# Kernel optimization log

Hardware: AMD Instinct MI355X
Metric: run time of the kernel (lower is better)

The kernel has to match this reference:

```python
import jax, jax.numpy as jnp
import numpy as np

EPS = 1e-12  # F.normalize default eps

def setup_inputs() -> dict:
    key = jax.random.key(0)
    k1, k2, k3, k4, k5, k6 = jax.random.split(key, 6)
    B, N, F_in, F_out = 8, 2048, 128, 128
    h = jax.random.normal(k1, (B, N, F_in), dtype=jnp.float32)
    # binary adjacency with avg degree ~32 (p = 32/2048)
    adj = (jax.random.uniform(k2, (B, N, N)) < (32.0 / N)).astype(jnp.float32)
    lim = 1.0 / np.sqrt(F_in)
    W_self = jax.random.uniform(k3, (F_in, F_out), minval=-lim, maxval=lim, dtype=jnp.float32)
    b_self = jax.random.uniform(k4, (F_out,), minval=-lim, maxval=lim, dtype=jnp.float32)
    W_neigh = jax.random.uniform(k5, (F_in, F_out), minval=-lim, maxval=lim, dtype=jnp.float32)
    b_neigh = jax.random.uniform(k6, (F_out,), minval=-lim, maxval=lim, dtype=jnp.float32)
    return {"h": h, "adj": adj, "W_self": W_self, "b_self": b_self,
            "W_neigh": W_neigh, "b_neigh": b_neigh}

def reference(h, adj, W_self, b_self, W_neigh, b_neigh):
    # Original builds (B,N,N,F) = adj[:, i, :, None] * h then mean over dim=-2.
    # mean divides by N (not degree), so aggregated = (adj @ h) / N. Fused form:
    N = h.shape[1]
    aggregated = jnp.einsum('bij,bjf->bif', adj, h) / N  # (B,N,F_in)
    out = h @ W_self + b_self + aggregated @ W_neigh + b_neigh
    out = jax.nn.relu(out)
    # F.normalize(p=2, dim=-1): x / max(||x||, eps)
    norm = jnp.linalg.norm(out, axis=-1, keepdims=True)
    out = out / jnp.maximum(norm, EPS)
    return out  # dropout(p=0.0) is identity
```

## Files before the change

### kernel.cpp

```cpp
#include <hip/hip_runtime.h>

typedef unsigned int u32;
typedef unsigned long long u64;
typedef float f4v __attribute__((ext_vector_type(4)));
typedef float f2v __attribute__((ext_vector_type(2)));

#define BATCH 8
#define NNODE 2048
#define FEAT  128
#define CAP   320


#define APITCH 68
#define BPITCH 132

__global__ __launch_bounds__(256) void gemm_pg_kernel(
    const float* __restrict__ h,
    const float* __restrict__ Ws,
    const float* __restrict__ bs,
    const float* __restrict__ Wn,
    const float* __restrict__ bn,
    float* __restrict__ P,
    float* __restrict__ G)
{
  __shared__ float sA[64 * APITCH];
  __shared__ float sB[64 * BPITCH];

  const int tid = threadIdx.x;
  const int tx = tid & 15;
  const int rg = tid >> 4;
  const int r0 = blockIdx.x * 64;
  const int half = blockIdx.y;
  const float* __restrict__ W = half ? Wn : Ws;
  float* __restrict__ op = half ? G : P;

  float acc[4][8];
#pragma unroll
  for (int r = 0; r < 4; r++)
#pragma unroll
    for (int c = 0; c < 8; c++) acc[r][c] = 0.0f;

  const int arl = tid >> 2;
  const int aq  = tid & 3;
  const int bkl = tid >> 2;
  const int bq  = tid & 3;

  for (int t = 0; t < 2; t++) {
    __syncthreads();
    {
      const float* src = h + (size_t)(r0 + arl) * FEAT + t * 64 + aq * 4;
#pragma unroll
      for (int ii = 0; ii < 4; ii++) {
        float4 vv = *(const float4*)(src + ii * 16);
        int kk = aq * 4 + ii * 16;
        sA[(kk + 0) * APITCH + arl] = vv.x;
        sA[(kk + 1) * APITCH + arl] = vv.y;
        sA[(kk + 2) * APITCH + arl] = vv.z;
        sA[(kk + 3) * APITCH + arl] = vv.w;
      }
    }
    {
      const float* src = W + (size_t)(t * 64 + bkl) * FEAT;
#pragma unroll
      for (int j = 0; j < 8; j++) {
        int cw = (bq + 4 * j) * 4;
        *(float4*)&sB[bkl * BPITCH + cw] = *(const float4*)(src + cw);
      }
    }
    __syncthreads();
#pragma unroll 4
    for (int k = 0; k < 64; k++) {
      float4 av = *(const float4*)&sA[k * APITCH + rg * 4];
      float4 b0 = *(const float4*)&sB[k * BPITCH + tx * 8];
      float4 b1 = *(const float4*)&sB[k * BPITCH + tx * 8 + 4];
      const float a[4] = {av.x, av.y, av.z, av.w};
      const float bb[8] = {b0.x, b0.y, b0.z, b0.w, b1.x, b1.y, b1.z, b1.w};
#pragma unroll
      for (int r = 0; r < 4; r++)
#pragma unroll
        for (int c = 0; c < 8; c++)
          acc[r][c] += a[r] * bb[c];
    }
  }

  float bias[8];
  if (half == 0) {
    float4 b0 = *(const float4*)(bs + tx * 8);
    float4 b1 = *(const float4*)(bs + tx * 8 + 4);
    float4 c0 = *(const float4*)(bn + tx * 8);
    float4 c1 = *(const float4*)(bn + tx * 8 + 4);
    bias[0] = b0.x + c0.x; bias[1] = b0.y + c0.y;
    bias[2] = b0.z + c0.z; bias[3] = b0.w + c0.w;
    bias[4] = b1.x + c1.x; bias[5] = b1.y + c1.y;
    bias[6] = b1.z + c1.z; bias[7] = b1.w + c1.w;
  } else {
#pragma unroll
    for (int c = 0; c < 8; c++) bias[c] = 0.0f;
  }
#pragma unroll
  for (int r = 0; r < 4; r++) {
    float* orow = op + (size_t)(r0 + rg * 4 + r) * FEAT + tx * 8;
    float4 w0, w1;
    w0.x = acc[r][0] + bias[0]; w0.y = acc[r][1] + bias[1];
    w0.z = acc[r][2] + bias[2]; w0.w = acc[r][3] + bias[3];
    w1.x = acc[r][4] + bias[4]; w1.y = acc[r][5] + bias[5];
    w1.z = acc[r][6] + bias[6]; w1.w = acc[r][7] + bias[7];
    *(float4*)(orow) = w0;
    *(float4*)(orow + 4) = w1;
  }
}

__global__ __launch_bounds__(256) void fused_agg_kernel(
    const float* __restrict__ adj,
    const float* __restrict__ G,
    const float* __restrict__ P,
    float* __restrict__ out)
{
  __shared__ int sIdx[4][CAP];
  const int tid = threadIdx.x;
  const int l = tid & 63;
  const int w = tid >> 6;
  const int row = blockIdx.x * 4 + w;
  const int b = row >> 11;
  const float* arow = adj + (size_t)row * NNODE;
  const float* gB = G + (size_t)b * NNODE * FEAT;
  const int l2 = 2 * l;
  int* idx = sIdx[w];

  const float2 pv = *(const float2*)(P + (size_t)row * FEAT + l2);

  f4v vc[8];
#pragma unroll
  for (int i = 0; i < 8; i++)
    vc[i] = __builtin_nontemporal_load((const f4v*)(arow + i * 256 + l * 4));

  u32 mask = 0;
#pragma unroll
  for (int i = 0; i < 8; i++) {
    mask |= (vc[i].x != 0.0f ? 1u : 0u) << (i * 4 + 0);
    mask |= (vc[i].y != 0.0f ? 1u : 0u) << (i * 4 + 1);
    mask |= (vc[i].z != 0.0f ? 1u : 0u) << (i * 4 + 2);
    mask |= (vc[i].w != 0.0f ? 1u : 0u) << (i * 4 + 3);
  }
  const int cnt = __popc(mask);
  int s = cnt;
#pragma unroll
  for (int d = 1; d < 64; d <<= 1) {
    int t = __shfl_up(s, d);
    if (l >= d) s += t;
  }
  const int total = __shfl(s, 63);
  int pos = s - cnt;
  u32 m = mask;
  while (m) {
    int bb = __builtin_ctz(m);
    m &= m - 1;
    if (pos < CAP) idx[pos] = ((bb >> 2) << 8) + 4 * l + (bb & 3);
    pos++;
  }
  const int n = (total < CAP) ? total : CAP;

  float ax = 0.0f, ay = 0.0f;
  int i = 0;
  for (; i + 8 <= n; i += 8) {
    int4 j0 = *(const int4*)&idx[i];
    int4 j1 = *(const int4*)&idx[i + 4];
    float2 g0 = *(const float2*)(gB + (size_t)j0.x * FEAT + l2);
    float2 g1 = *(const float2*)(gB + (size_t)j0.y * FEAT + l2);
    float2 g2 = *(const float2*)(gB + (size_t)j0.z * FEAT + l2);
    float2 g3 = *(const float2*)(gB + (size_t)j0.w * FEAT + l2);
    float2 g4 = *(const float2*)(gB + (size_t)j1.x * FEAT + l2);
    float2 g5 = *(const float2*)(gB + (size_t)j1.y * FEAT + l2);
    float2 g6 = *(const float2*)(gB + (size_t)j1.z * FEAT + l2);
    float2 g7 = *(const float2*)(gB + (size_t)j1.w * FEAT + l2);
    ax += ((g0.x + g1.x) + (g2.x + g3.x)) + ((g4.x + g5.x) + (g6.x + g7.x));
    ay += ((g0.y + g1.y) + (g2.y + g3.y)) + ((g4.y + g5.y) + (g6.y + g7.y));
  }
  for (; i < n; i++) {
    int j = idx[i];
    const float2 g = *(const float2*)(gB + (size_t)j * FEAT + l2);
    ax += g.x; ay += g.y;
  }

  const float invN = 1.0f / (float)NNODE;
  float px = pv.x + ax * invN;
  float py = pv.y + ay * invN;
  px = px > 0.0f ? px : 0.0f;
  py = py > 0.0f ? py : 0.0f;

  float ssum = px * px + py * py;
  ssum += __shfl_xor(ssum, 1);
  ssum += __shfl_xor(ssum, 2);
  ssum += __shfl_xor(ssum, 4);
  ssum += __shfl_xor(ssum, 8);
  ssum += __shfl_xor(ssum, 16);
  ssum += __shfl_xor(ssum, 32);
  float nrm = sqrtf(ssum);
  if (nrm < 1e-12f) nrm = 1e-12f;
  const float inv = 1.0f / nrm;

  f2v res;
  res.x = px * inv;
  res.y = py * inv;
  __builtin_nontemporal_store(res, (f2v*)(out + (size_t)row * FEAT + l2));
}

extern "C" void kernel_launch(void* const* d_in, const int* in_sizes, int n_in,
                              void* d_out, int out_size, void* d_ws, size_t ws_size,
                              hipStream_t stream) {
  const float* h   = (const float*)d_in[0];
  const float* adj = (const float*)d_in[1];
  const float* Ws  = (const float*)d_in[2];
  const float* bs  = (const float*)d_in[3];
  const float* Wn  = (const float*)d_in[4];
  const float* bn  = (const float*)d_in[5];
  float* out = (float*)d_out;
  float* P = (float*)d_ws;
  float* G = P + (size_t)BATCH * NNODE * FEAT;

  (void)in_sizes; (void)n_in; (void)out_size; (void)ws_size;

  gemm_pg_kernel<<<dim3(BATCH * NNODE / 64, 2), dim3(256), 0, stream>>>(
      h, Ws, bs, Wn, bn, P, G);
  fused_agg_kernel<<<dim3(BATCH * NNODE / 4), dim3(256), 0, stream>>>(
      adj, G, P, out);
}
```

Baseline: 228.3 us.

## Move adjacency scan into GEMM kernel and pass neighbor lists to gather kernel

The adjacency-row scan that builds neighbor index lists now runs as extra blocks of the first kernel, alongside the dense P/G GEMM tiles, instead of inside the aggregation kernel. The lists and counts go to workspace memory (capacity reduced to 96 per row), so the second kernel only loads them and gathers rows of G. The large adjacency read therefore no longer waits behind the GEMM. The gather kernel also swizzles block order so concurrently running blocks spread across batches. The cost is an extra global round trip for the index lists, and rows with more than 96 neighbors would be truncated.

```diff
diff --git a/kernel.cpp b/kernel.cpp
--- a/kernel.cpp
+++ b/kernel.cpp
@@ -8,29 +8,75 @@
 #define BATCH 8
 #define NNODE 2048
 #define FEAT  128
-#define CAP   320
+#define LCAP  96
 
 
 #define APITCH 68
 #define BPITCH 132
-
-__global__ __launch_bounds__(256) void gemm_pg_kernel(
+#define NGEMM  512
+
+__global__ __launch_bounds__(256) void fused_k1(
     const float* __restrict__ h,
     const float* __restrict__ Ws,
     const float* __restrict__ bs,
     const float* __restrict__ Wn,
     const float* __restrict__ bn,
+    const float* __restrict__ adj,
     float* __restrict__ P,
-    float* __restrict__ G)
+    float* __restrict__ G,
+    int* __restrict__ cnt,
+    int* __restrict__ lst)
 {
   __shared__ float sA[64 * APITCH];
   __shared__ float sB[64 * BPITCH];
 
   const int tid = threadIdx.x;
+  const int bid = blockIdx.x;
+
+  if (bid >= NGEMM) {
+    const int l = tid & 63;
+    const int w = tid >> 6;
+    const int row = (bid - NGEMM) * 4 + w;
+    const float* arow = adj + (size_t)row * NNODE;
+
+    f4v vc[8];
+#pragma unroll
+    for (int i = 0; i < 8; i++)
+      vc[i] = __builtin_nontemporal_load((const f4v*)(arow + i * 256 + l * 4));
+
+    u32 mask = 0;
+#pragma unroll
+    for (int i = 0; i < 8; i++) {
+      mask |= (vc[i].x != 0.0f ? 1u : 0u) << (i * 4 + 0);
+      mask |= (vc[i].y != 0.0f ? 1u : 0u) << (i * 4 + 1);
+      mask |= (vc[i].z != 0.0f ? 1u : 0u) << (i * 4 + 2);
+      mask |= (vc[i].w != 0.0f ? 1u : 0u) << (i * 4 + 3);
+    }
+    const int c_ = __popc(mask);
+    int s = c_;
+#pragma unroll
+    for (int d = 1; d < 64; d <<= 1) {
+      int t = __shfl_up(s, d);
+      if (l >= d) s += t;
+    }
+    const int total = __shfl(s, 63);
+    int pos = s - c_;
+    u32 m = mask;
+    int* lrow = lst + (size_t)row * LCAP;
+    while (m) {
+      int bb = __builtin_ctz(m);
+      m &= m - 1;
+      if (pos < LCAP) lrow[pos] = ((bb >> 2) << 8) + 4 * l + (bb & 3);
+      pos++;
+    }
+    if (l == 0) cnt[row] = (total < LCAP) ? total : LCAP;
+    return;
+  }
+
   const int tx = tid & 15;
   const int rg = tid >> 4;
-  const int r0 = blockIdx.x * 64;
-  const int half = blockIdx.y;
+  const int half = bid & 1;
+  const int r0 = (bid >> 1) * 64;
   const float* __restrict__ W = half ? Wn : Ws;
   float* __restrict__ op = half ? G : P;
 
@@ -110,55 +156,31 @@
   }
 }
 
-__global__ __launch_bounds__(256) void fused_agg_kernel(
-    const float* __restrict__ adj,
+__global__ __launch_bounds__(256) void gather_k2(
     const float* __restrict__ G,
     const float* __restrict__ P,
+    const int* __restrict__ cnt,
+    const int* __restrict__ lst,
     float* __restrict__ out)
 {
-  __shared__ int sIdx[4][CAP];
+  __shared__ int sIdx[4][LCAP];
   const int tid = threadIdx.x;
   const int l = tid & 63;
   const int w = tid >> 6;
-  const int row = blockIdx.x * 4 + w;
+  const int bid = blockIdx.x;
+  const int sw = (bid & 7) * 512 + (bid >> 3);
+  const int row = sw * 4 + w;
   const int b = row >> 11;
-  const float* arow = adj + (size_t)row * NNODE;
   const float* gB = G + (size_t)b * NNODE * FEAT;
   const int l2 = 2 * l;
   int* idx = sIdx[w];
 
   const float2 pv = *(const float2*)(P + (size_t)row * FEAT + l2);
-
-  f4v vc[8];
-#pragma unroll
-  for (int i = 0; i < 8; i++)
-    vc[i] = __builtin_nontemporal_load((const f4v*)(arow + i * 256 + l * 4));
-
-  u32 mask = 0;
-#pragma unroll
-  for (int i = 0; i < 8; i++) {
-    mask |= (vc[i].x != 0.0f ? 1u : 0u) << (i * 4 + 0);
-    mask |= (vc[i].y != 0.0f ? 1u : 0u) << (i * 4 + 1);
-    mask |= (vc[i].z != 0.0f ? 1u : 0u) << (i * 4 + 2);
-    mask |= (vc[i].w != 0.0f ? 1u : 0u) << (i * 4 + 3);
-  }
-  const int cnt = __popc(mask);
-  int s = cnt;
-#pragma unroll
-  for (int d = 1; d < 64; d <<= 1) {
-    int t = __shfl_up(s, d);
-    if (l >= d) s += t;
-  }
-  const int total = __shfl(s, 63);
-  int pos = s - cnt;
-  u32 m = mask;
-  while (m) {
-    int bb = __builtin_ctz(m);
-    m &= m - 1;
-    if (pos < CAP) idx[pos] = ((bb >> 2) << 8) + 4 * l + (bb & 3);
-    pos++;
-  }
-  const int n = (total < CAP) ? total : CAP;
+  const int n = cnt[row];
+  const int* lrow = lst + (size_t)row * LCAP;
+  idx[l] = lrow[l];
+  if (l < LCAP - 64) idx[64 + l] = lrow[64 + l];
+  __syncthreads();
 
   float ax = 0.0f, ay = 0.0f;
   int i = 0;
@@ -215,13 +237,16 @@
   const float* Wn  = (const float*)d_in[4];
   const float* bn  = (const float*)d_in[5];
   float* out = (float*)d_out;
+
   float* P = (float*)d_ws;
   float* G = P + (size_t)BATCH * NNODE * FEAT;
+  int* cnt = (int*)(G + (size_t)BATCH * NNODE * FEAT);
+  int* lst = cnt + (size_t)BATCH * NNODE;
 
   (void)in_sizes; (void)n_in; (void)out_size; (void)ws_size;
 
-  gemm_pg_kernel<<<dim3(BATCH * NNODE / 64, 2), dim3(256), 0, stream>>>(
-      h, Ws, bs, Wn, bn, P, G);
-  fused_agg_kernel<<<dim3(BATCH * NNODE / 4), dim3(256), 0, stream>>>(
-      adj, G, P, out);
+  fused_k1<<<dim3(NGEMM + BATCH * NNODE / 4), dim3(256), 0, stream>>>(
+      h, Ws, bs, Wn, bn, adj, P, G, cnt, lst);
+  gather_k2<<<dim3(BATCH * NNODE / 4), dim3(256), 0, stream>>>(
+      G, P, cnt, lst, out);
 }
```

Result: no change. 231.9 us (+1.6%).
